# Optimization experiments

Measured on AMD Instinct MI355X. Metric: run time of the kernel, lower is better.

The kernel has to match this reference:

```python
import jax, jax.numpy as jnp
import numpy as np
from jax import lax

MIN_TRACK_LEN = 20

def setup_inputs() -> dict:
    key = jax.random.key(0)
    k1, k2 = jax.random.split(key)
    B, F, T, NB = 16, 257, 8000, 64
    mag = jax.random.uniform(k1, (B, F, T), dtype=jnp.float32)          # magnitude spectrogram, >= 0
    freq_fb = jax.random.uniform(k2, (NB, F), dtype=jnp.float32)        # band filterbank
    return {
        "mag": mag,
        "freq_fb": freq_fb,
        "noise_scale": jnp.array(1.5, dtype=jnp.float32),
        "raw_rise": jnp.array(-1.5, dtype=jnp.float32),
        "raw_fall": jnp.array(-3.0, dtype=jnp.float32),
    }

def reference(mag, freq_fb, noise_scale, raw_rise, raw_fall):
    rise = jax.nn.sigmoid(raw_rise)
    fall = jax.nn.sigmoid(raw_fall)
    T = mag.shape[2]
    # initial noise floor from first min_track_len frames: (B, F)
    init_min = jnp.clip(jnp.min(mag[:, :, :min(MIN_TRACK_LEN, T)], axis=2), 1e-5, None)
    floor_min = init_min * 0.5

    def step(noise_floor, frame):  # noise_floor, frame: (B, F)
        alpha = jnp.where(frame > noise_floor, rise, fall)
        nf = (1.0 - alpha) * noise_floor + alpha * frame
        nf = jnp.maximum(nf, floor_min)
        return nf, nf

    _, noise_t = lax.scan(step, init_min, jnp.moveaxis(mag, 2, 0))  # (T, B, F)
    running_noise = jnp.moveaxis(noise_t, 0, 2)                      # (B, F, T)

    vnr = mag / (jnp.abs(noise_scale) * running_noise + 1e-8)        # (B, F, T)
    vnr_bands = jnp.tanh(jnp.einsum('nf,bft->bnt', freq_fb, vnr) / 10.0)
    return jnp.nan_to_num(vnr_bands, nan=0.0, posinf=1.0, neginf=0.0)
```

## Files before the change

### kernel.cpp

```cpp
#include <hip/hip_runtime.h>
#include <stdint.h>

#define B_      16
#define F_      257
#define T_      8000
#define NB_     64
#define TT_     64
#define NTILES  125
#define TPC     2
#define NCHUNK  64
#define WTILES  2

typedef __attribute__((ext_vector_type(8))) short short8;
typedef __attribute__((ext_vector_type(4))) float floatx4;

__device__ __forceinline__ unsigned short f2bf(float x) {
    union { float f; unsigned u; } v; v.f = x;
    unsigned r = v.u + 0x7FFFu + ((v.u >> 16) & 1u);
    return (unsigned short)(r >> 16);
}
__device__ __forceinline__ float bf2f(unsigned short h) {
    union { float f; unsigned u; } v; v.u = ((unsigned)h) << 16;
    return v.f;
}

__device__ __forceinline__ int stidx(int t, int f) {
    const int st = ((t & 3) << 2) | ((t >> 2) & 3);
    return t * 256 + (f ^ (st << 3));
}

__global__ __launch_bounds__(256, 4) void vnr_fused_kernel(
    const float* __restrict__ mag, const float* __restrict__ fb,
    const float* __restrict__ p_ns, const float* __restrict__ p_rr,
    const float* __restrict__ p_rf, float* __restrict__ out)
{
    __shared__ unsigned short tile16[64 * 256];
    __shared__ float mag256s[64];
    __shared__ float vnr256s[64];

    const int tid  = threadIdx.x;
    const int lane = tid & 63;
    const int w    = tid >> 6;
    const int l15  = tid & 15;
    const int q    = (tid & 63) >> 4;

    const int bid = blockIdx.x;
    const int b   = bid & 15;
    const int c   = bid >> 4;

    const float ns   = fabsf(p_ns[0]);
    const float rise = 1.0f / (1.0f + __expf(-p_rr[0]));
    const float fall = 1.0f / (1.0f + __expf(-p_rf[0]));

    const float* magp = mag + (size_t)b * (size_t)F_ * (size_t)T_;

    short8 afrag[8];
    {
        const float* fbrow = fb + (16 * w + l15) * F_;
        #pragma unroll
        for (int kt = 0; kt < 8; ++kt) {
            const int f0 = 32 * kt + 8 * q;
            short8 a;
            #pragma unroll
            for (int j = 0; j < 8; ++j) a[j] = (short)f2bf(fbrow[f0 + j]);
            afrag[kt] = a;
        }
    }
    float fb256[4];
    #pragma unroll
    for (int r = 0; r < 4; ++r) fb256[r] = fb[(16 * w + 4 * q + r) * F_ + 256];

    const int f_own = tid;
    float mn = 1e30f;
    #pragma unroll
    for (int t = 0; t < 20; ++t) mn = fminf(mn, magp[(size_t)f_own * T_ + t]);
    const float initv  = fmaxf(mn, 1e-5f);
    const float floorv = 0.5f * initv;
    float nf = initv;

    float nf256 = 0.f, floor256 = 0.f;
    if (tid == 0) {
        float m2 = 1e30f;
        for (int t = 0; t < 20; ++t) m2 = fminf(m2, magp[(size_t)256 * T_ + t]);
        float iv = fmaxf(m2, 1e-5f);
        nf256 = iv; floor256 = 0.5f * iv;
    }

    const int bodyBeg = TPC * c;
    const int tileBeg = (c == 0) ? 0 : max(0, bodyBeg - WTILES);
    const int tileEnd = min(bodyBeg + TPC, NTILES);

    for (int tile = tileBeg; tile < tileEnd; ++tile) {
        const bool body = (tile >= bodyBeg);
        const int t0 = tile * TT_;

        __syncthreads();
        #pragma unroll 4
        for (int i = 0; i < 8; ++i) {
            const int p = i * 16 + (tid >> 4);
            const int s = tid & 15;
            const float4 ga = *(const float4*)&magp[(size_t)(2 * p)     * T_ + (t0 + 4 * s)];
            const float4 gb = *(const float4*)&magp[(size_t)(2 * p + 1) * T_ + (t0 + 4 * s)];
            #pragma unroll
            for (int k = 0; k < 4; ++k) {
                const int t = 4 * s + k;
                const float xa = (&ga.x)[k];
                const float xb = (&gb.x)[k];
                const unsigned pack = (unsigned)f2bf(xa) | ((unsigned)f2bf(xb) << 16);
                *(unsigned*)&tile16[stidx(t, 2 * p)] = pack;
            }
        }
        if (w == 0) mag256s[lane] = magp[(size_t)256 * T_ + (t0 + lane)];
        __syncthreads();

        {
            float nfl = nf;
            if (body) {
                #pragma unroll
                for (int jb = 0; jb < 64; jb += 16) {
                    unsigned short xs[16];
                    #pragma unroll
                    for (int u = 0; u < 16; ++u)
                        xs[u] = tile16[stidx(jb + u, f_own)];
                    #pragma unroll
                    for (int u = 0; u < 16; ++u) {
                        const float x = bf2f(xs[u]);
                        const float a = (x > nfl) ? rise : fall;
                        nfl = fmaxf(__builtin_fmaf(a, x - nfl, nfl), floorv);
                        const float vnr = x * __builtin_amdgcn_rcpf(ns * nfl + 1e-8f);
                        tile16[stidx(jb + u, f_own)] = f2bf(vnr);
                    }
                }
            } else {
                #pragma unroll
                for (int jb = 0; jb < 64; jb += 16) {
                    unsigned short xs[16];
                    #pragma unroll
                    for (int u = 0; u < 16; ++u)
                        xs[u] = tile16[stidx(jb + u, f_own)];
                    #pragma unroll
                    for (int u = 0; u < 16; ++u) {
                        const float x = bf2f(xs[u]);
                        const float a = (x > nfl) ? rise : fall;
                        nfl = fmaxf(__builtin_fmaf(a, x - nfl, nfl), floorv);
                    }
                }
            }
            nf = nfl;
            if (tid == 0) {
                float nl = nf256;
                for (int j = 0; j < 64; ++j) {
                    const float x = mag256s[j];
                    const float a = (x > nl) ? rise : fall;
                    nl = fmaxf(__builtin_fmaf(a, x - nl, nl), floor256);
                    if (body) vnr256s[j] = x * __builtin_amdgcn_rcpf(ns * nl + 1e-8f);
                }
                nf256 = nl;
            }
        }
        if (!body) continue;
        __syncthreads();

        const int stl3 = ((((l15 & 3) << 2) | (l15 >> 2)) << 3);
        floatx4 acc[4];
        #pragma unroll
        for (int tt = 0; tt < 4; ++tt) acc[tt] = (floatx4){0.f, 0.f, 0.f, 0.f};

        #pragma unroll
        for (int kt = 0; kt < 8; ++kt) {
            #pragma unroll
            for (int tt = 0; tt < 4; ++tt) {
                const int t = tt * 16 + l15;
                const short8* bp = (const short8*)
                    &tile16[t * 256 + ((32 * kt + 8 * q) ^ stl3)];
                acc[tt] = __builtin_amdgcn_mfma_f32_16x16x32_bf16(afrag[kt], *bp, acc[tt], 0, 0, 0);
            }
        }

        const size_t outb = (size_t)b * NB_ * T_;
        #pragma unroll
        for (int tt = 0; tt < 4; ++tt) {
            const int t = tt * 16 + l15;
            const float v256 = vnr256s[t];
            #pragma unroll
            for (int r = 0; r < 4; ++r) {
                const float s = acc[tt][r] + fb256[r] * v256;
                const float e = __expf(s * 0.2f);
                const float y = 1.0f - 2.0f * __builtin_amdgcn_rcpf(e + 1.0f);
                out[outb + (size_t)(16 * w + 4 * q + r) * T_ + (size_t)(t0 + t)] = y;
            }
        }
    }
}

extern "C" void kernel_launch(void* const* d_in, const int* in_sizes, int n_in,
                              void* d_out, int out_size, void* d_ws, size_t ws_size,
                              hipStream_t stream) {
    (void)in_sizes; (void)n_in; (void)d_ws; (void)ws_size; (void)out_size;
    const float* mag = (const float*)d_in[0];
    const float* fb  = (const float*)d_in[1];
    const float* ns  = (const float*)d_in[2];
    const float* rr  = (const float*)d_in[3];
    const float* rf  = (const float*)d_in[4];
    float* out = (float*)d_out;

    dim3 grid(B_ * NCHUNK);
    dim3 block(256);
    hipLaunchKernelGGL(vnr_fused_kernel, grid, block, 0, stream, mag, fb, ns, rr, rf, out);
}
```

Measured before the change: 250.3 us.

## Load each frequency row directly into registers and drop LDS staging for recursion

Each thread now reads its own frequency row of the magnitude tile from global memory as float4 vectors into registers. It runs the noise-floor recursion in fp32 on those registers instead of first staging a bf16 tile in shared memory. Warm-up tiles no longer touch shared memory or issue barriers, and the bin-256 recursion is spread across waves by block index and unrolled. The aim is to cut barrier, LDS-store and bf16 packing overhead. The cost is that loads are no longer coalesced across lanes (each lane reads a different row) and register pressure rises from holding 64 floats per thread.

```diff
diff --git a/kernel.cpp b/kernel.cpp
--- a/kernel.cpp
+++ b/kernel.cpp
@@ -19,10 +19,6 @@
     unsigned r = v.u + 0x7FFFu + ((v.u >> 16) & 1u);
     return (unsigned short)(r >> 16);
 }
-__device__ __forceinline__ float bf2f(unsigned short h) {
-    union { float f; unsigned u; } v; v.u = ((unsigned)h) << 16;
-    return v.f;
-}
 
 __device__ __forceinline__ int stidx(int t, int f) {
     const int st = ((t & 3) << 2) | ((t >> 2) & 3);
@@ -47,12 +43,15 @@
     const int bid = blockIdx.x;
     const int b   = bid & 15;
     const int c   = bid >> 4;
+    const int hw  = bid & 3;
 
     const float ns   = fabsf(p_ns[0]);
     const float rise = 1.0f / (1.0f + __expf(-p_rr[0]));
     const float fall = 1.0f / (1.0f + __expf(-p_rf[0]));
 
-    const float* magp = mag + (size_t)b * (size_t)F_ * (size_t)T_;
+    const float* magp   = mag + (size_t)b * (size_t)F_ * (size_t)T_;
+    const float* rowp   = magp + (size_t)tid * (size_t)T_;
+    const float* row256 = magp + (size_t)256 * (size_t)T_;
 
     short8 afrag[8];
     {
@@ -70,124 +69,134 @@
     #pragma unroll
     for (int r = 0; r < 4; ++r) fb256[r] = fb[(16 * w + 4 * q + r) * F_ + 256];
 
-    const int f_own = tid;
     float mn = 1e30f;
     #pragma unroll
-    for (int t = 0; t < 20; ++t) mn = fminf(mn, magp[(size_t)f_own * T_ + t]);
+    for (int u = 0; u < 5; ++u) {
+        const float4 v = *(const float4*)&rowp[4 * u];
+        mn = fminf(mn, fminf(fminf(v.x, v.y), fminf(v.z, v.w)));
+    }
     const float initv  = fmaxf(mn, 1e-5f);
     const float floorv = 0.5f * initv;
     float nf = initv;
 
+    const bool isH = (tid == (hw << 6));
     float nf256 = 0.f, floor256 = 0.f;
-    if (tid == 0) {
+    if (isH) {
         float m2 = 1e30f;
-        for (int t = 0; t < 20; ++t) m2 = fminf(m2, magp[(size_t)256 * T_ + t]);
+        #pragma unroll
+        for (int u = 0; u < 5; ++u) {
+            const float4 v = *(const float4*)&row256[4 * u];
+            m2 = fminf(m2, fminf(fminf(v.x, v.y), fminf(v.z, v.w)));
+        }
         float iv = fmaxf(m2, 1e-5f);
         nf256 = iv; floor256 = 0.5f * iv;
     }
 
     const int bodyBeg = TPC * c;
-    const int tileBeg = (c == 0) ? 0 : max(0, bodyBeg - WTILES);
+    const int tileBeg = (c == 0) ? 0 : bodyBeg - WTILES;
     const int tileEnd = min(bodyBeg + TPC, NTILES);
 
     for (int tile = tileBeg; tile < tileEnd; ++tile) {
-        const bool body = (tile >= bodyBeg);
         const int t0 = tile * TT_;
 
-        __syncthreads();
-        #pragma unroll 4
-        for (int i = 0; i < 8; ++i) {
-            const int p = i * 16 + (tid >> 4);
-            const int s = tid & 15;
-            const float4 ga = *(const float4*)&magp[(size_t)(2 * p)     * T_ + (t0 + 4 * s)];
-            const float4 gb = *(const float4*)&magp[(size_t)(2 * p + 1) * T_ + (t0 + 4 * s)];
-            #pragma unroll
-            for (int k = 0; k < 4; ++k) {
-                const int t = 4 * s + k;
-                const float xa = (&ga.x)[k];
-                const float xb = (&gb.x)[k];
-                const unsigned pack = (unsigned)f2bf(xa) | ((unsigned)f2bf(xb) << 16);
-                *(unsigned*)&tile16[stidx(t, 2 * p)] = pack;
-            }
-        }
-        if (w == 0) mag256s[lane] = magp[(size_t)256 * T_ + (t0 + lane)];
-        __syncthreads();
-
-        {
-            float nfl = nf;
-            if (body) {
-                #pragma unroll
-                for (int jb = 0; jb < 64; jb += 16) {
-                    unsigned short xs[16];
-                    #pragma unroll
-                    for (int u = 0; u < 16; ++u)
-                        xs[u] = tile16[stidx(jb + u, f_own)];
-                    #pragma unroll
-                    for (int u = 0; u < 16; ++u) {
-                        const float x = bf2f(xs[u]);
+        float4 xs[16];
+        #pragma unroll
+        for (int u = 0; u < 16; ++u)
+            xs[u] = *(const float4*)&rowp[t0 + 4 * u];
+        if (w == hw) mag256s[lane] = row256[t0 + lane];
+
+        if (tile >= bodyBeg) {
+            __syncthreads();
+            {
+                float nfl = nf;
+                #pragma unroll
+                for (int u = 0; u < 16; ++u) {
+                    #pragma unroll
+                    for (int k = 0; k < 4; ++k) {
+                        const float x = (&xs[u].x)[k];
                         const float a = (x > nfl) ? rise : fall;
                         nfl = fmaxf(__builtin_fmaf(a, x - nfl, nfl), floorv);
                         const float vnr = x * __builtin_amdgcn_rcpf(ns * nfl + 1e-8f);
-                        tile16[stidx(jb + u, f_own)] = f2bf(vnr);
+                        tile16[stidx(4 * u + k, tid)] = f2bf(vnr);
                     }
                 }
-            } else {
+                nf = nfl;
+            }
+            if (isH) {
+                float nl = nf256;
                 #pragma unroll
                 for (int jb = 0; jb < 64; jb += 16) {
-                    unsigned short xs[16];
-                    #pragma unroll
-                    for (int u = 0; u < 16; ++u)
-                        xs[u] = tile16[stidx(jb + u, f_own)];
-                    #pragma unroll
-                    for (int u = 0; u < 16; ++u) {
-                        const float x = bf2f(xs[u]);
-                        const float a = (x > nfl) ? rise : fall;
-                        nfl = fmaxf(__builtin_fmaf(a, x - nfl, nfl), floorv);
+                    float xv[16];
+                    #pragma unroll
+                    for (int u2 = 0; u2 < 16; ++u2) xv[u2] = mag256s[jb + u2];
+                    #pragma unroll
+                    for (int u2 = 0; u2 < 16; ++u2) {
+                        const float x = xv[u2];
+                        const float a2 = (x > nl) ? rise : fall;
+                        nl = fmaxf(__builtin_fmaf(a2, x - nl, nl), floor256);
+                        vnr256s[jb + u2] = x * __builtin_amdgcn_rcpf(ns * nl + 1e-8f);
                     }
                 }
-            }
-            nf = nfl;
-            if (tid == 0) {
-                float nl = nf256;
-                for (int j = 0; j < 64; ++j) {
-                    const float x = mag256s[j];
-                    const float a = (x > nl) ? rise : fall;
-                    nl = fmaxf(__builtin_fmaf(a, x - nl, nl), floor256);
-                    if (body) vnr256s[j] = x * __builtin_amdgcn_rcpf(ns * nl + 1e-8f);
-                }
                 nf256 = nl;
             }
-        }
-        if (!body) continue;
-        __syncthreads();
-
-        const int stl3 = ((((l15 & 3) << 2) | (l15 >> 2)) << 3);
-        floatx4 acc[4];
-        #pragma unroll
-        for (int tt = 0; tt < 4; ++tt) acc[tt] = (floatx4){0.f, 0.f, 0.f, 0.f};
-
-        #pragma unroll
-        for (int kt = 0; kt < 8; ++kt) {
+            __syncthreads();
+
+            const int stl3 = ((((l15 & 3) << 2) | (l15 >> 2)) << 3);
+            floatx4 acc[4];
+            #pragma unroll
+            for (int tt = 0; tt < 4; ++tt) acc[tt] = (floatx4){0.f, 0.f, 0.f, 0.f};
+
+            #pragma unroll
+            for (int kt = 0; kt < 8; ++kt) {
+                #pragma unroll
+                for (int tt = 0; tt < 4; ++tt) {
+                    const int t = tt * 16 + l15;
+                    const short8* bp = (const short8*)
+                        &tile16[t * 256 + ((32 * kt + 8 * q) ^ stl3)];
+                    acc[tt] = __builtin_amdgcn_mfma_f32_16x16x32_bf16(afrag[kt], *bp, acc[tt], 0, 0, 0);
+                }
+            }
+
+            const size_t outb = (size_t)b * NB_ * T_;
             #pragma unroll
             for (int tt = 0; tt < 4; ++tt) {
                 const int t = tt * 16 + l15;
-                const short8* bp = (const short8*)
-                    &tile16[t * 256 + ((32 * kt + 8 * q) ^ stl3)];
-                acc[tt] = __builtin_amdgcn_mfma_f32_16x16x32_bf16(afrag[kt], *bp, acc[tt], 0, 0, 0);
-            }
-        }
-
-        const size_t outb = (size_t)b * NB_ * T_;
-        #pragma unroll
-        for (int tt = 0; tt < 4; ++tt) {
-            const int t = tt * 16 + l15;
-            const float v256 = vnr256s[t];
-            #pragma unroll
-            for (int r = 0; r < 4; ++r) {
-                const float s = acc[tt][r] + fb256[r] * v256;
-                const float e = __expf(s * 0.2f);
-                const float y = 1.0f - 2.0f * __builtin_amdgcn_rcpf(e + 1.0f);
-                out[outb + (size_t)(16 * w + 4 * q + r) * T_ + (size_t)(t0 + t)] = y;
+                const float v256 = vnr256s[t];
+                #pragma unroll
+                for (int r = 0; r < 4; ++r) {
+                    const float s = acc[tt][r] + fb256[r] * v256;
+                    const float e = __expf(s * 0.2f);
+                    const float y = 1.0f - 2.0f * __builtin_amdgcn_rcpf(e + 1.0f);
+                    out[outb + (size_t)(16 * w + 4 * q + r) * T_ + (size_t)(t0 + t)] = y;
+                }
+            }
+        } else {
+            float nfl = nf;
+            #pragma unroll
+            for (int u = 0; u < 16; ++u) {
+                #pragma unroll
+                for (int k = 0; k < 4; ++k) {
+                    const float x = (&xs[u].x)[k];
+                    const float a = (x > nfl) ? rise : fall;
+                    nfl = fmaxf(__builtin_fmaf(a, x - nfl, nfl), floorv);
+                }
+            }
+            nf = nfl;
+            if (isH) {
+                float nl = nf256;
+                #pragma unroll
+                for (int jb = 0; jb < 64; jb += 16) {
+                    float xv[16];
+                    #pragma unroll
+                    for (int u2 = 0; u2 < 16; ++u2) xv[u2] = mag256s[jb + u2];
+                    #pragma unroll
+                    for (int u2 = 0; u2 < 16; ++u2) {
+                        const float x = xv[u2];
+                        const float a2 = (x > nl) ? rise : fall;
+                        nl = fmaxf(__builtin_fmaf(a2, x - nl, nl), floor256);
+                    }
+                }
+                nf256 = nl;
             }
         }
     }
```

Result: slower. 262.1 us (+4.7%).
